# Kernel tuning notes

Hardware: AMD Instinct MI355X
Metric: run time of the kernel (lower is better)

The kernel has to match this reference:

```python
import jax, jax.numpy as jnp
import numpy as np

N = 16384
E = 262144
HID = 128
NFILT = 128
NGAUSS = 50
NINTER = 6
CUTOFF = 10.0
NUMZ = 100
LOG2 = 0.6931471805599453


def ssp(x):
    # ShiftedSoftplus
    return jax.nn.softplus(x) - LOG2


def setup_inputs() -> dict:
    key = jax.random.key(0)
    ks = jax.random.split(key, 20)
    z = jax.random.randint(ks[0], (N,), 0, NUMZ)
    pos = jax.random.uniform(ks[1], (N, 3), dtype=jnp.float32) * 5.0  # box side 5 -> all pairs < cutoff
    edge_index = jax.random.randint(ks[2], (2, E), 0, N)
    s = lambda k, shape, fan: jax.random.normal(k, shape, dtype=jnp.float32) / np.sqrt(fan)
    params = dict(
        emb=s(ks[3], (NUMZ, HID), 1.0),
        Wf1=s(ks[4], (NINTER, NGAUSS, NFILT), NGAUSS), bf1=jnp.zeros((NINTER, NFILT), jnp.float32),
        Wf2=s(ks[5], (NINTER, NFILT, NFILT), NFILT), bf2=jnp.zeros((NINTER, NFILT), jnp.float32),
        Wl1=s(ks[6], (NINTER, HID, NFILT), HID),
        Wl2=s(ks[7], (NINTER, NFILT, HID), NFILT), bl2=jnp.zeros((NINTER, HID), jnp.float32),
        Wl=s(ks[8], (NINTER, HID, HID), HID), bl=jnp.zeros((NINTER, HID), jnp.float32),
        Wo1=s(ks[9], (HID, HID // 2), HID), bo1=jnp.zeros((HID // 2,), jnp.float32),
        Wo2=s(ks[10], (HID // 2, 1), HID // 2), bo2=jnp.zeros((1,), jnp.float32),
    )
    return dict(z=z, pos=pos, edge_index=edge_index, **params)


def reference(z, pos, edge_index, emb, Wf1, bf1, Wf2, bf2, Wl1, Wl2, bl2, Wl, bl, Wo1, bo1, Wo2, bo2):
    src, dst = edge_index[0], edge_index[1]
    # edge distances and Gaussian smearing
    d = jnp.linalg.norm(pos[src] - pos[dst], axis=-1)          # [E]
    offset = jnp.linspace(0.0, CUTOFF, NGAUSS, dtype=jnp.float32)
    coeff = -0.5 / (offset[1] - offset[0]) ** 2
    ea = jnp.exp(coeff * (d[:, None] - offset) ** 2)            # [E, NGAUSS]
    C = 0.5 * (jnp.cos(d * (np.pi / CUTOFF)) + 1.0)             # cosine cutoff [E]

    h = emb[z]                                                  # [N, HID]
    for i in range(NINTER):
        # continuous-filter weights
        Wfilt = (ssp(ea @ Wf1[i] + bf1[i]) @ Wf2[i] + bf2[i]) * C[:, None]  # [E, NFILT]
        x = h @ Wl1[i]                                          # lin1, no bias [N, NFILT]
        msg = x[src] * Wfilt                                    # gather + filter
        agg = jax.ops.segment_sum(msg, dst, num_segments=N)     # scatter-sum [N, NFILT]
        x = ssp(agg @ Wl2[i] + bl2[i]) @ Wl[i] + bl[i]          # lin2 -> ssp -> lin
        h = h + x

    h = ssp(h @ Wo1 + bo1) @ Wo2 + bo2                          # [N, 1] per-atom energy
    out = jnp.sum(h, axis=0, keepdims=True)                     # 'add' readout, single graph -> [1, 1]
    return jax.nn.relu(out)
```

## Files before the change

### kernel.cpp

```cpp
#include <hip/hip_runtime.h>
#include <math.h>

#define NATOM 16384
#define NEDGE 262144
#define HID 128
#define NG 50
#define NI 6

typedef _Float16 h8_t __attribute__((ext_vector_type(8)));
typedef _Float16 h4_t __attribute__((ext_vector_type(4)));
typedef float    f4_t __attribute__((ext_vector_type(4)));

__device__ __forceinline__ float ssp_f(float v) {
    float e = __expf(-fabsf(v));
    return fmaxf(v, 0.0f) + __logf(1.0f + e) - 0.69314718055994531f;
}

__global__ void fill0(float* __restrict__ p, int n4) {
    int i = blockIdx.x * 256 + threadIdx.x;
    if (i < n4) ((float4*)p)[i] = make_float4(0.f, 0.f, 0.f, 0.f);
}

__global__ void hist_k(const int* __restrict__ ei, int* __restrict__ cnt) {
    int e = blockIdx.x * 256 + threadIdx.x;
    if (e < NEDGE) atomicAdd(&cnt[ei[NEDGE + e]], 1);
}

__global__ void scan_k(const int* __restrict__ cnt, int* __restrict__ offs) {
    __shared__ int part[256];
    int t = threadIdx.x;
    int base = t * 64;
    int s = 0;
    for (int i = 0; i < 64; ++i) s += cnt[base + i];
    part[t] = s;
    __syncthreads();
    for (int off = 1; off < 256; off <<= 1) {
        int v = (t >= off) ? part[t - off] : 0;
        __syncthreads();
        part[t] += v;
        __syncthreads();
    }
    int r = part[t] - s;
    for (int i = 0; i < 64; ++i) { offs[base + i] = r; r += cnt[base + i]; }
    if (t == 255) offs[NATOM] = r;
}

__global__ void scatter_k(const int* __restrict__ ei, const int* __restrict__ offs,
                          int* __restrict__ cnt, int* __restrict__ sSrc, int* __restrict__ sDst) {
    int e = blockIdx.x * 256 + threadIdx.x;
    if (e >= NEDGE) return;
    int d = ei[NEDGE + e];
    int r = atomicAdd(&cnt[d], 1);
    int j = offs[d] + r;
    sSrc[j] = ei[e];
    sDst[j] = d;
}

__global__ void edge_pre(const float* __restrict__ pos,
                         const int* __restrict__ sSrc, const int* __restrict__ sDst,
                         _Float16* __restrict__ ea, float* __restrict__ Cb) {
    int j = blockIdx.x * 256 + threadIdx.x;
    if (j >= NEDGE) return;
    int s = sSrc[j], dd = sDst[j];
    float dx = pos[3*s]   - pos[3*dd];
    float dy = pos[3*s+1] - pos[3*dd+1];
    float dz = pos[3*s+2] - pos[3*dd+2];
    float d = sqrtf(dx*dx + dy*dy + dz*dz);
    Cb[j] = 0.5f * (cosf(d * 0.31415926535897931f) + 1.0f);
    const float delta = 10.0f / 49.0f;
    const float coeff = -0.5f / (delta * delta);
    #pragma unroll
    for (int gq = 0; gq < 8; ++gq) {
        h8_t hv;
        #pragma unroll
        for (int r = 0; r < 8; ++r) {
            int g = gq * 8 + r;
            float v = 0.0f;
            if (g < NG) { float u = d - (float)g * delta; v = __expf(coeff * u * u); }
            hv[r] = (_Float16)v;
        }
        *(h8_t*)&ea[(size_t)j * 64 + gq * 8] = hv;
    }
}

__global__ void wprep(const float* __restrict__ Wf1, const float* __restrict__ Wf2,
                      const float* __restrict__ Wl1, const float* __restrict__ Wl2,
                      const float* __restrict__ Wl,
                      _Float16* __restrict__ w1, _Float16* __restrict__ w2,
                      _Float16* __restrict__ wn) {
    int idx = blockIdx.x * 256 + threadIdx.x;
    const int S1 = NI * 128 * 64, S2 = NI * 128 * 128;
    if (idx < S1) {
        int i = idx >> 13, r = idx & 8191, fo = r >> 6, k = r & 63;
        float v = (k < NG) ? Wf1[(size_t)i * NG * 128 + k * 128 + fo] : 0.0f;
        w1[idx] = (_Float16)v;
        return;
    }
    idx -= S1;
    if (idx < S2) {
        int i = idx >> 14, r = idx & 16383, fo = r >> 7, k = r & 127;
        w2[idx] = (_Float16)Wf2[(size_t)i * 128 * 128 + k * 128 + fo];
        return;
    }
    idx -= S2;
    if (idx < 3 * S2) {
        int mi = idx >> 14;
        int r = idx & 16383, fo = r >> 7, k = r & 127;
        int m = mi / NI, i = mi % NI;
        const float* W = (m == 0) ? Wl1 : (m == 1) ? Wl2 : Wl;
        wn[idx] = (_Float16)W[(size_t)i * 128 * 128 + k * 128 + fo];
    }
}

__global__ void embed_k(const int* __restrict__ z, const float* __restrict__ emb,
                        float* __restrict__ h) {
    int tid = blockIdx.x * 256 + threadIdx.x;
    int n = tid >> 7, f = tid & 127;
    h[tid] = emb[z[n] * HID + f];
}

__launch_bounds__(256)
__global__ void gemm_node_mfma(const float* __restrict__ A,
                               const _Float16* __restrict__ wt,
                               _Float16* __restrict__ xh) {
    __shared__ _Float16 aS[64 * 136];
    int t = threadIdx.x;
    int mb = blockIdx.x * 64;
    #pragma unroll
    for (int j = 0; j < 8; ++j) {
        int idx = t + j * 256;
        int row = idx >> 5, c4 = idx & 31;
        f4_t v = *(const f4_t*)&A[(size_t)(mb + row) * HID + c4 * 4];
        h4_t hh;
        #pragma unroll
        for (int r = 0; r < 4; ++r) hh[r] = (_Float16)v[r];
        *(h4_t*)&aS[row * 136 + c4 * 4] = hh;
    }
    __syncthreads();

    int wv = t >> 6, lane = t & 63, l15 = lane & 15, quad = lane >> 4;
    f4_t acc[2][4];
    #pragma unroll
    for (int m = 0; m < 2; ++m)
        #pragma unroll
        for (int n = 0; n < 4; ++n) acc[m][n] = (f4_t)0.0f;

    for (int kc = 0; kc < 4; ++kc) {
        int k0 = kc * 32 + quad * 8;
        h8_t a[2];
        #pragma unroll
        for (int m = 0; m < 2; ++m)
            a[m] = *(const h8_t*)&wt[(wv * 32 + m * 16 + l15) * 128 + k0];
        #pragma unroll
        for (int n = 0; n < 4; ++n) {
            h8_t b = *(const h8_t*)&aS[(n * 16 + l15) * 136 + k0];
            #pragma unroll
            for (int m = 0; m < 2; ++m)
                acc[m][n] = __builtin_amdgcn_mfma_f32_16x16x32_f16(a[m], b, acc[m][n], 0, 0, 0);
        }
    }

    #pragma unroll
    for (int n = 0; n < 4; ++n) {
        int el = n * 16 + l15;
        size_t row = (size_t)(mb + el);
        #pragma unroll
        for (int m = 0; m < 2; ++m) {
            int fb = wv * 32 + m * 16 + quad * 4;
            h4_t o;
            #pragma unroll
            for (int r = 0; r < 4; ++r) o[r] = (_Float16)acc[m][n][r];
            *(h4_t*)&xh[row * 128 + fb] = o;
        }
    }
}

__launch_bounds__(256)
__global__ void gemm_node3(const float* __restrict__ agg,
                           const _Float16* __restrict__ w2t, const _Float16* __restrict__ wlt,
                           const _Float16* __restrict__ w1n,
                           const float* __restrict__ bl2, const float* __restrict__ bl,
                           float* __restrict__ h, _Float16* __restrict__ xh) {
    __shared__ _Float16 aS[64 * 136];
    int t = threadIdx.x;
    int mb = blockIdx.x * 64;
    #pragma unroll
    for (int j = 0; j < 8; ++j) {
        int idx = t + j * 256;
        int row = idx >> 5, c4 = idx & 31;
        f4_t v = *(const f4_t*)&agg[(size_t)(mb + row) * HID + c4 * 4];
        h4_t hh;
        #pragma unroll
        for (int r = 0; r < 4; ++r) hh[r] = (_Float16)v[r];
        *(h4_t*)&aS[row * 136 + c4 * 4] = hh;
    }
    __syncthreads();

    int wv = t >> 6, lane = t & 63, l15 = lane & 15, quad = lane >> 4;
    int fq = wv * 32 + quad * 4;
    f4_t acc[2][4];

    #pragma unroll
    for (int m = 0; m < 2; ++m)
        #pragma unroll
        for (int n = 0; n < 4; ++n) acc[m][n] = (f4_t)0.0f;
    for (int kc = 0; kc < 4; ++kc) {
        int k0 = kc * 32 + quad * 8;
        h8_t a[2];
        #pragma unroll
        for (int m = 0; m < 2; ++m)
            a[m] = *(const h8_t*)&w2t[(wv * 32 + m * 16 + l15) * 128 + k0];
        #pragma unroll
        for (int n = 0; n < 4; ++n) {
            h8_t b = *(const h8_t*)&aS[(n * 16 + l15) * 136 + k0];
            #pragma unroll
            for (int m = 0; m < 2; ++m)
                acc[m][n] = __builtin_amdgcn_mfma_f32_16x16x32_f16(a[m], b, acc[m][n], 0, 0, 0);
        }
    }
    f4_t b2v[2];
    b2v[0] = *(const f4_t*)&bl2[fq]; b2v[1] = *(const f4_t*)&bl2[fq + 16];
    __syncthreads();

    #pragma unroll
    for (int m = 0; m < 2; ++m)
        #pragma unroll
        for (int n = 0; n < 4; ++n) {
            int el = n * 16 + l15;
            int fb = wv * 32 + m * 16 + quad * 4;
            h4_t hh;
            #pragma unroll
            for (int r = 0; r < 4; ++r)
                hh[r] = (_Float16)ssp_f(acc[m][n][r] + b2v[m][r]);
            *(h4_t*)&aS[el * 136 + fb] = hh;
        }
    __syncthreads();

    #pragma unroll
    for (int m = 0; m < 2; ++m)
        #pragma unroll
        for (int n = 0; n < 4; ++n) acc[m][n] = (f4_t)0.0f;
    for (int kc = 0; kc < 4; ++kc) {
        int k0 = kc * 32 + quad * 8;
        h8_t a[2];
        #pragma unroll
        for (int m = 0; m < 2; ++m)
            a[m] = *(const h8_t*)&wlt[(wv * 32 + m * 16 + l15) * 128 + k0];
        #pragma unroll
        for (int n = 0; n < 4; ++n) {
            h8_t b = *(const h8_t*)&aS[(n * 16 + l15) * 136 + k0];
            #pragma unroll
            for (int m = 0; m < 2; ++m)
                acc[m][n] = __builtin_amdgcn_mfma_f32_16x16x32_f16(a[m], b, acc[m][n], 0, 0, 0);
        }
    }
    f4_t blv[2];
    blv[0] = *(const f4_t*)&bl[fq]; blv[1] = *(const f4_t*)&bl[fq + 16];
    __syncthreads();

    #pragma unroll
    for (int n = 0; n < 4; ++n) {
        int el = n * 16 + l15;
        size_t row = (size_t)(mb + el);
        #pragma unroll
        for (int m = 0; m < 2; ++m) {
            int fb = wv * 32 + m * 16 + quad * 4;
            f4_t hv = *(const f4_t*)&h[row * 128 + fb];
            f4_t o;
            h4_t hh;
            #pragma unroll
            for (int r = 0; r < 4; ++r) {
                o[r] = hv[r] + acc[m][n][r] + blv[m][r];
                hh[r] = (_Float16)o[r];
            }
            *(f4_t*)&h[row * 128 + fb] = o;
            *(h4_t*)&aS[el * 136 + fb] = hh;
        }
    }
    if (!w1n) return;
    __syncthreads();

    #pragma unroll
    for (int m = 0; m < 2; ++m)
        #pragma unroll
        for (int n = 0; n < 4; ++n) acc[m][n] = (f4_t)0.0f;
    for (int kc = 0; kc < 4; ++kc) {
        int k0 = kc * 32 + quad * 8;
        h8_t a[2];
        #pragma unroll
        for (int m = 0; m < 2; ++m)
            a[m] = *(const h8_t*)&w1n[(wv * 32 + m * 16 + l15) * 128 + k0];
        #pragma unroll
        for (int n = 0; n < 4; ++n) {
            h8_t b = *(const h8_t*)&aS[(n * 16 + l15) * 136 + k0];
            #pragma unroll
            for (int m = 0; m < 2; ++m)
                acc[m][n] = __builtin_amdgcn_mfma_f32_16x16x32_f16(a[m], b, acc[m][n], 0, 0, 0);
        }
    }
    #pragma unroll
    for (int n = 0; n < 4; ++n) {
        int el = n * 16 + l15;
        size_t row = (size_t)(mb + el);
        #pragma unroll
        for (int m = 0; m < 2; ++m) {
            int fb = wv * 32 + m * 16 + quad * 4;
            h4_t o;
            #pragma unroll
            for (int r = 0; r < 4; ++r) o[r] = (_Float16)acc[m][n][r];
            *(h4_t*)&xh[row * 128 + fb] = o;
        }
    }
}

#define T1_LDW 136
#define EA_LDW 72
#define NDST 16

__launch_bounds__(256, 3)
__global__ void edge_filter(const _Float16* __restrict__ xh, float* __restrict__ agg,
                            const int* __restrict__ sSrc, const int* __restrict__ sDst,
                            const int* __restrict__ offs, const float* __restrict__ Cb,
                            const _Float16* __restrict__ ea,
                            const _Float16* __restrict__ w1, const _Float16* __restrict__ w2,
                            const float* __restrict__ bf1, const float* __restrict__ bf2) {
    __shared__ __align__(16) _Float16 eaS[64 * EA_LDW];
    __shared__ __align__(16) _Float16 t1S[64 * T1_LDW];
    __shared__ float accS[NDST * 128];
    __shared__ int dstl[64];

    _Float16* msg = t1S;

    int t = threadIdx.x;
    int wv = t >> 6, lane = t & 63;
    int l15 = lane & 15, quad = lane >> 4;
    int d0 = blockIdx.x * NDST;
    int estart = offs[d0];
    int ecnt = offs[d0 + NDST] - estart;
    int tmax = (ecnt + 63) >> 6;

    #pragma unroll
    for (int c = 0; c < 2; ++c)
        *(f4_t*)&accS[(t + c * 256) * 4] = (f4_t)0.0f;

    h8_t w1f[2][2], w2f[4][2];
    #pragma unroll
    for (int kc = 0; kc < 2; ++kc) {
        int k0 = kc * 32 + quad * 8;
        #pragma unroll
        for (int m = 0; m < 2; ++m)
            w1f[kc][m] = *(const h8_t*)&w1[(wv * 32 + m * 16 + l15) * 64 + k0];
    }
    #pragma unroll
    for (int kc = 0; kc < 4; ++kc) {
        int k0 = kc * 32 + quad * 8;
        #pragma unroll
        for (int m = 0; m < 2; ++m)
            w2f[kc][m] = *(const h8_t*)&w2[(wv * 32 + m * 16 + l15) * 128 + k0];
    }
    int fq = wv * 32 + quad * 4;
    f4_t b1v[2], b2v[2];
    b1v[0] = *(const f4_t*)&bf1[fq];  b1v[1] = *(const f4_t*)&bf1[fq + 16];
    b2v[0] = *(const f4_t*)&bf2[fq];  b2v[1] = *(const f4_t*)&bf2[fq + 16];

    for (int tt = 0; tt < tmax; ++tt) {
        int base = estart + tt * 64;
        int lim = ecnt - tt * 64;

        #pragma unroll
        for (int c = 0; c < 2; ++c) {
            int ch = t + c * 256;
            int e = ch >> 3, ks = ch & 7;
            h8_t v = (h8_t)(_Float16)0.0f;
            if (e < lim) v = *(const h8_t*)&ea[(size_t)(base + e) * 64 + ks * 8];
            *(h8_t*)&eaS[e * EA_LDW + ks * 8] = v;
        }
        if (t < 64) {
            int dl = 0;
            if (t < lim) dl = sDst[base + t] - d0;
            dstl[t] = dl;
        }
        int srcn[4];
        float cn[4];
        #pragma unroll
        for (int n = 0; n < 4; ++n) {
            int rel = n * 16 + l15;
            bool ok = rel < lim;
            srcn[n] = ok ? sSrc[base + rel] : 0;
            cn[n]   = ok ? Cb[base + rel] : 0.0f;
        }
        h4_t xr[4][2];
        #pragma unroll
        for (int n = 0; n < 4; ++n)
            #pragma unroll
            for (int m = 0; m < 2; ++m)
                xr[n][m] = *(const h4_t*)&xh[(size_t)srcn[n] * HID + wv * 32 + m * 16 + quad * 4];
        __syncthreads();

        f4_t acc1[2][4];
        #pragma unroll
        for (int m = 0; m < 2; ++m)
            #pragma unroll
            for (int n = 0; n < 4; ++n) acc1[m][n] = (f4_t)0.0f;
        #pragma unroll
        for (int kc = 0; kc < 2; ++kc) {
            int k0 = kc * 32 + quad * 8;
            h8_t b[4];
            #pragma unroll
            for (int n = 0; n < 4; ++n)
                b[n] = *(const h8_t*)&eaS[(n * 16 + l15) * EA_LDW + k0];
            #pragma unroll
            for (int m = 0; m < 2; ++m)
                #pragma unroll
                for (int n = 0; n < 4; ++n)
                    acc1[m][n] = __builtin_amdgcn_mfma_f32_16x16x32_f16(w1f[kc][m], b[n], acc1[m][n], 0, 0, 0);
        }

        #pragma unroll
        for (int m = 0; m < 2; ++m)
            #pragma unroll
            for (int n = 0; n < 4; ++n) {
                int el = n * 16 + l15;
                int fb = wv * 32 + m * 16 + quad * 4;
                h4_t hh;
                #pragma unroll
                for (int r = 0; r < 4; ++r)
                    hh[r] = (_Float16)ssp_f(acc1[m][n][r] + b1v[m][r]);
                *(h4_t*)&t1S[el * T1_LDW + fb] = hh;
            }
        __syncthreads();

        f4_t acc2[2][4];
        #pragma unroll
        for (int m = 0; m < 2; ++m)
            #pragma unroll
            for (int n = 0; n < 4; ++n) acc2[m][n] = (f4_t)0.0f;
        #pragma unroll
        for (int kc = 0; kc < 4; ++kc) {
            int k0 = kc * 32 + quad * 8;
            #pragma unroll
            for (int n = 0; n < 4; ++n) {
                h8_t b = *(const h8_t*)&t1S[(n * 16 + l15) * T1_LDW + k0];
                #pragma unroll
                for (int m = 0; m < 2; ++m)
                    acc2[m][n] = __builtin_amdgcn_mfma_f32_16x16x32_f16(w2f[kc][m], b, acc2[m][n], 0, 0, 0);
            }
        }
        __syncthreads();

        #pragma unroll
        for (int n = 0; n < 4; ++n) {
            int el = n * 16 + l15;
            float ce = cn[n];
            #pragma unroll
            for (int m = 0; m < 2; ++m) {
                int fb = wv * 32 + m * 16 + quad * 4;
                h4_t o;
                #pragma unroll
                for (int r = 0; r < 4; ++r)
                    o[r] = (_Float16)((acc2[m][n][r] + b2v[m][r]) * ce * (float)xr[n][m][r]);
                *(h4_t*)&msg[el * T1_LDW + fb] = o;
            }
        }
        __syncthreads();

        {
            int f = t & 127, hf = t >> 7;
            int ib = hf * 32;
            float run = 0.0f;
            int cur = dstl[ib];
            for (int i = ib; i < ib + 32; ++i) {
                int dnow = dstl[i];
                if (dnow != cur) {
                    atomicAdd(&accS[cur * 128 + f], run);
                    run = 0.0f;
                    cur = dnow;
                }
                run += (float)msg[i * T1_LDW + f];
            }
            atomicAdd(&accS[cur * 128 + f], run);
        }
        __syncthreads();
    }

    float* dstp = &agg[(size_t)d0 * HID];
    #pragma unroll
    for (int c = 0; c < 2; ++c) {
        int idx = t + c * 256;
        *(f4_t*)&dstp[idx * 4] = *(const f4_t*)&accS[idx * 4];
    }
}

__launch_bounds__(256)
__global__ void readout1(const float* __restrict__ h, const float* __restrict__ Wo1,
                         const float* __restrict__ bo1, const float* __restrict__ Wo2,
                         const float* __restrict__ bo2, float* __restrict__ accum) {
    __shared__ float w1[128 * 64];
    __shared__ float part[4];
    int t = threadIdx.x;
    for (int i = t; i < 128 * 16; i += 256)
        ((float4*)w1)[i] = ((const float4*)Wo1)[i];
    __syncthreads();
    int f = t & 63, wv = t >> 6;
    float b = bo1[f], w2v = Wo2[f];
    float lsum = 0.0f;
    for (int a = 0; a < 16; ++a) {
        int n = blockIdx.x * 64 + wv * 16 + a;
        const float* hr = &h[(size_t)n * HID];
        float acc = b;
        #pragma unroll 16
        for (int k = 0; k < 128; ++k)
            acc = fmaf(hr[k], w1[k*64 + f], acc);
        lsum += ssp_f(acc) * w2v;
    }
    #pragma unroll
    for (int off = 32; off > 0; off >>= 1)
        lsum += __shfl_down(lsum, off, 64);
    if (f == 0) part[wv] = lsum;
    __syncthreads();
    if (t == 0)
        atomicAdd(accum, part[0] + part[1] + part[2] + part[3] + 64.0f * bo2[0]);
}

__global__ void readout2(const float* __restrict__ accum, float* __restrict__ out) {
    out[0] = fmaxf(accum[0], 0.0f);
}

extern "C" void kernel_launch(void* const* d_in, const int* in_sizes, int n_in,
                              void* d_out, int out_size, void* d_ws, size_t ws_size,
                              hipStream_t stream) {
    const int*   z   = (const int*)d_in[0];
    const float* pos = (const float*)d_in[1];
    const int*   ei  = (const int*)d_in[2];
    const float* emb = (const float*)d_in[3];
    const float* Wf1 = (const float*)d_in[4];
    const float* bf1 = (const float*)d_in[5];
    const float* Wf2 = (const float*)d_in[6];
    const float* bf2 = (const float*)d_in[7];
    const float* Wl1 = (const float*)d_in[8];
    const float* Wl2 = (const float*)d_in[9];
    const float* bl2 = (const float*)d_in[10];
    const float* Wl  = (const float*)d_in[11];
    const float* bl  = (const float*)d_in[12];
    const float* Wo1 = (const float*)d_in[13];
    const float* bo1 = (const float*)d_in[14];
    const float* Wo2 = (const float*)d_in[15];
    const float* bo2 = (const float*)d_in[16];
    float* out = (float*)d_out;

    _Float16* w1 = (_Float16*)d_ws;
    _Float16* w2 = w1 + NI * 8192;
    _Float16* wn = w2 + NI * 16384;
    _Float16* ea = wn + 3 * NI * 16384;
    _Float16* xh = ea + (size_t)NEDGE * 64;
    float* Cb  = (float*)(xh + (size_t)NATOM * 128);
    float* h   = Cb + NEDGE;
    float* agg = h + (size_t)NATOM * HID;
    float* accum = agg + (size_t)NATOM * HID;
    int* cnt  = (int*)(accum + 4);
    int* offs = cnt + NATOM;
    int* sSrc = offs + NATOM + 4;
    int* sDst = sSrc + NEDGE;

    fill0<<<NATOM/4/256, 256, 0, stream>>>((float*)cnt, NATOM/4);
    hist_k<<<NEDGE/256, 256, 0, stream>>>(ei, cnt);
    scan_k<<<1, 256, 0, stream>>>(cnt, offs);
    fill0<<<NATOM/4/256, 256, 0, stream>>>((float*)cnt, NATOM/4);
    scatter_k<<<NEDGE/256, 256, 0, stream>>>(ei, offs, cnt, sSrc, sDst);

    edge_pre<<<NEDGE/256, 256, 0, stream>>>(pos, sSrc, sDst, ea, Cb);
    wprep<<<(NI*8192 + NI*16384 + 3*NI*16384)/256, 256, 0, stream>>>(
        Wf1, Wf2, Wl1, Wl2, Wl, w1, w2, wn);
    embed_k<<<(NATOM*HID)/256, 256, 0, stream>>>(z, emb, h);

    gemm_node_mfma<<<NATOM/64, 256, 0, stream>>>(h, wn, xh);
    for (int i = 0; i < NI; ++i) {
        edge_filter<<<NATOM/NDST, 256, 0, stream>>>(xh, agg, sSrc, sDst, offs, Cb, ea,
            w1 + (size_t)i*8192, w2 + (size_t)i*16384,
            bf1 + i*HID, bf2 + i*HID);
        const _Float16* w1n = (i < NI-1) ? wn + (size_t)(i+1)*16384 : nullptr;
        gemm_node3<<<NATOM/64, 256, 0, stream>>>(agg,
            wn + (size_t)(1*NI+i)*16384, wn + (size_t)(2*NI+i)*16384,
            w1n, bl2 + i*HID, bl + i*HID, h, xh);
    }
    fill0<<<1, 256, 0, stream>>>(accum, 1);
    readout1<<<NATOM/64, 256, 0, stream>>>(h, Wo1, bo1, Wo2, bo2, accum);
    readout2<<<1, 1, 0, stream>>>(accum, out);
}
```

Baseline: 792.0 us.

## Accumulate edge messages directly into LDS with atomics instead of staged segmented reduce

The edge filter kernel no longer writes fp16 messages to shared memory and then runs a per-feature segmented reduction over destination indices. Each lane now adds its fp32 message values straight into a padded shared accumulator with LDS atomics. This removes two block barriers per tile and the staging buffer, and occupancy is raised from 3 to 4 blocks per CU. Because edges are sorted by destination, lanes in a wave often hit the same address, so the atomics may serialize heavily.

After: 2.113 ms. 2.67x slower.

```diff
diff --git a/kernel.cpp b/kernel.cpp
--- a/kernel.cpp
+++ b/kernel.cpp
@@ -316,8 +316,9 @@
 #define T1_LDW 136
 #define EA_LDW 72
 #define NDST 16
-
-__launch_bounds__(256, 3)
+#define ACC_LDW 132
+
+__launch_bounds__(256, 4)
 __global__ void edge_filter(const _Float16* __restrict__ xh, float* __restrict__ agg,
                             const int* __restrict__ sSrc, const int* __restrict__ sDst,
                             const int* __restrict__ offs, const float* __restrict__ Cb,
@@ -326,10 +327,7 @@
                             const float* __restrict__ bf1, const float* __restrict__ bf2) {
     __shared__ __align__(16) _Float16 eaS[64 * EA_LDW];
     __shared__ __align__(16) _Float16 t1S[64 * T1_LDW];
-    __shared__ float accS[NDST * 128];
-    __shared__ int dstl[64];
-
-    _Float16* msg = t1S;
+    __shared__ float accS[NDST * ACC_LDW];
 
     int t = threadIdx.x;
     int wv = t >> 6, lane = t & 63;
@@ -339,9 +337,8 @@
     int ecnt = offs[d0 + NDST] - estart;
     int tmax = (ecnt + 63) >> 6;
 
-    #pragma unroll
-    for (int c = 0; c < 2; ++c)
-        *(f4_t*)&accS[(t + c * 256) * 4] = (f4_t)0.0f;
+    for (int i = t; i < NDST * ACC_LDW / 4; i += 256)
+        *(f4_t*)&accS[i * 4] = (f4_t)0.0f;
 
     h8_t w1f[2][2], w2f[4][2];
     #pragma unroll
@@ -375,18 +372,14 @@
             if (e < lim) v = *(const h8_t*)&ea[(size_t)(base + e) * 64 + ks * 8];
             *(h8_t*)&eaS[e * EA_LDW + ks * 8] = v;
         }
-        if (t < 64) {
-            int dl = 0;
-            if (t < lim) dl = sDst[base + t] - d0;
-            dstl[t] = dl;
-        }
-        int srcn[4];
+        int srcn[4], dstn[4];
         float cn[4];
         #pragma unroll
         for (int n = 0; n < 4; ++n) {
             int rel = n * 16 + l15;
             bool ok = rel < lim;
             srcn[n] = ok ? sSrc[base + rel] : 0;
+            dstn[n] = ok ? (sDst[base + rel] - d0) : 0;
             cn[n]   = ok ? Cb[base + rel] : 0.0f;
         }
         h4_t xr[4][2];
@@ -450,44 +443,23 @@
 
         #pragma unroll
         for (int n = 0; n < 4; ++n) {
-            int el = n * 16 + l15;
             float ce = cn[n];
+            int db = dstn[n] * ACC_LDW;
             #pragma unroll
             for (int m = 0; m < 2; ++m) {
                 int fb = wv * 32 + m * 16 + quad * 4;
-                h4_t o;
                 #pragma unroll
                 for (int r = 0; r < 4; ++r)
-                    o[r] = (_Float16)((acc2[m][n][r] + b2v[m][r]) * ce * (float)xr[n][m][r]);
-                *(h4_t*)&msg[el * T1_LDW + fb] = o;
+                    atomicAdd(&accS[db + fb + r],
+                              (acc2[m][n][r] + b2v[m][r]) * ce * (float)xr[n][m][r]);
             }
         }
-        __syncthreads();
-
-        {
-            int f = t & 127, hf = t >> 7;
-            int ib = hf * 32;
-            float run = 0.0f;
-            int cur = dstl[ib];
-            for (int i = ib; i < ib + 32; ++i) {
-                int dnow = dstl[i];
-                if (dnow != cur) {
-                    atomicAdd(&accS[cur * 128 + f], run);
-                    run = 0.0f;
-                    cur = dnow;
-                }
-                run += (float)msg[i * T1_LDW + f];
-            }
-            atomicAdd(&accS[cur * 128 + f], run);
-        }
-        __syncthreads();
-    }
-
-    float* dstp = &agg[(size_t)d0 * HID];
-    #pragma unroll
-    for (int c = 0; c < 2; ++c) {
-        int idx = t + c * 256;
-        *(f4_t*)&dstp[idx * 4] = *(const f4_t*)&accS[idx * 4];
+    }
+    __syncthreads();
+
+    for (int i = t; i < NDST * 128 / 4; i += 256) {
+        int row = i >> 5, c4 = i & 31;
+        *(f4_t*)&agg[(size_t)(d0 + row) * HID + c4 * 4] = *(const f4_t*)&accS[row * ACC_LDW + c4 * 4];
     }
 }
 
```
